# Kernel tuning notes

Hardware: AMD Instinct MI355X
Metric: run time of the kernel (lower is better)

The kernel has to match this reference:

```python
import jax, jax.numpy as jnp
import numpy as np
import math

B, W, BINS, BANDS = 2, 2048, 1024, 8  # cropsize == W
HEAD = BINS // BANDS


def setup_inputs() -> dict:
    key = jax.random.key(0)
    ks = jax.random.split(key, 10)
    s = 1.0 / math.sqrt(BINS)
    return {
        "x": jax.random.normal(ks[0], (B, W, BINS), jnp.float32),
        "Wq": jax.random.normal(ks[1], (BINS, BINS), jnp.float32) * s,
        "bq": jax.random.normal(ks[2], (BINS,), jnp.float32) * s,
        "Wk": jax.random.normal(ks[3], (BINS, BINS), jnp.float32) * s,
        "bk": jax.random.normal(ks[4], (BINS,), jnp.float32) * s,
        "Wv": jax.random.normal(ks[5], (BINS, BINS), jnp.float32) * s,
        "bv": jax.random.normal(ks[6], (BINS,), jnp.float32) * s,
        "Wo": jax.random.normal(ks[7], (BINS, BINS), jnp.float32) * s,
        "bo": jax.random.normal(ks[8], (BINS,), jnp.float32) * s,
        "er": jax.random.normal(ks[9], (HEAD, W), jnp.float32) * s,  # [bins//num_bands, cropsize]
    }


def reference(x, Wq, bq, Wk, bk, Wv, bv, Wo, bo, er):
    b, w, h = x.shape
    n = BANDS
    # projections -> [b, n, w, head]
    q = (x @ Wq.T + bq).reshape(b, w, n, -1).transpose(0, 2, 1, 3)
    k = (x @ Wk.T + bk).reshape(b, w, n, -1).transpose(0, 2, 1, 3)
    v = (x @ Wv.T + bv).reshape(b, w, n, -1).transpose(0, 2, 1, 3)
    # relative position bias via skew trick: [b, n, w, cropsize]
    qer = jnp.einsum('bnwd,dc->bnwc', q, er)
    p = jnp.pad(qer, ((0, 0), (0, 0), (0, 0), (1, 0)))  # pad left of last dim
    p = jnp.swapaxes(p, 2, 3)[:, :, 1:, :]              # [b, n, w, w]
    a = (jnp.einsum('bnqd,bnkd->bnqk', q, k) + p) / math.sqrt(h)
    attn = jax.nn.softmax(a, axis=-1)
    ctx = jnp.einsum('bnqk,bnkd->bnqd', attn, v).transpose(0, 2, 1, 3).reshape(b, w, h)
    o = ctx @ Wo.T + bo
    return (o, a)
```

## Files before the change

### kernel.cpp

```cpp
#include <hip/hip_runtime.h>

typedef __attribute__((ext_vector_type(8))) __bf16 bf16x8;
typedef __attribute__((ext_vector_type(4))) float f32x4;

__device__ __forceinline__ unsigned short f2bf(float f) {
  __bf16 h = (__bf16)f;
  return __builtin_bit_cast(unsigned short, h);
}

__device__ __forceinline__ f32x4 mfma_bf16(bf16x8 a, bf16x8 b, f32x4 c) {
  return __builtin_amdgcn_mfma_f32_16x16x32_bf16(a, b, c, 0, 0, 0);
}

__device__ __forceinline__ void gload_lds16(const void* g, void* l) {
  __builtin_amdgcn_global_load_lds((const __attribute__((address_space(1))) void*)g,
                                   (__attribute__((address_space(3))) void*)l, 16, 0, 0);
}


__global__ void cvt_f32_bf16(const float* __restrict__ in, unsigned short* __restrict__ out, int n4) {
  int i = blockIdx.x * blockDim.x + threadIdx.x;
  if (i < n4) {
    float4 v = reinterpret_cast<const float4*>(in)[i];
    ushort4 o;
    o.x = f2bf(v.x); o.y = f2bf(v.y); o.z = f2bf(v.z); o.w = f2bf(v.w);
    reinterpret_cast<ushort4*>(out)[i] = o;
  }
}

__global__ void cvt4_f32_bf16(const float* __restrict__ a, const float* __restrict__ b,
                              const float* __restrict__ c, const float* __restrict__ d,
                              unsigned short* __restrict__ oa, unsigned short* __restrict__ ob,
                              unsigned short* __restrict__ oc, unsigned short* __restrict__ od) {
  int i = blockIdx.x * blockDim.x + threadIdx.x;
  int which = i >> 18, j = i & 262143;
  const float* src = (which == 0) ? a : (which == 1) ? b : (which == 2) ? c : d;
  unsigned short* dst = (which == 0) ? oa : (which == 1) ? ob : (which == 2) ? oc : od;
  float4 v = reinterpret_cast<const float4*>(src)[j];
  ushort4 o;
  o.x = f2bf(v.x); o.y = f2bf(v.y); o.z = f2bf(v.z); o.w = f2bf(v.w);
  reinterpret_cast<ushort4*>(dst)[j] = o;
}

__global__ void er_transpose(const float* __restrict__ er, unsigned short* __restrict__ ert) {
  __shared__ float t[32][33];
  int w0 = blockIdx.x * 32, d0 = blockIdx.y * 32;
  int tx = threadIdx.x, ty = threadIdx.y;
#pragma unroll
  for (int i = 0; i < 4; ++i)
    t[ty + i * 8][tx] = er[(size_t)(d0 + ty + i * 8) * 2048 + w0 + tx];
  __syncthreads();
#pragma unroll
  for (int i = 0; i < 4; ++i)
    ert[(size_t)(w0 + ty + i * 8) * 128 + d0 + tx] = f2bf(t[tx][ty + i * 8]);
}


__device__ __forceinline__ void gemm_tile(
    const unsigned short* __restrict__ A,
    const unsigned short* __restrict__ Bt,
    const float* __restrict__ bias,
    void* __restrict__ C,
    int mode, int i0, int j0,
    unsigned short* lds)
{
  char* base = (char*)lds;

  const int tid = threadIdx.x;
  const int lane = tid & 63, wid = tid >> 6;
  const int lr = lane & 15, lq = lane >> 4;
  const int wr = wid >> 1, wc = wid & 1;

  f32x4 acc[4][4] = {};

  const int srow = tid >> 2;
  const int scolb = (tid & 3) << 4;

  const char* Abase = (const char*)A + (size_t)(i0 + srow) * 2048 + scolb;
  const char* Bbase = (const char*)Bt + (size_t)(j0 + srow) * 2048 + scolb;

  gload_lds16(Abase,             base + tid * 16);
  gload_lds16(Abase + 64 * 2048, base + 4096 + tid * 16);
  gload_lds16(Bbase,             base + 8192 + tid * 16);
  gload_lds16(Bbase + 64 * 2048, base + 12288 + tid * 16);

  for (int kt = 0; kt < 32; ++kt) {
    char* cbuf = base + (kt & 1) * 16384;
    char* nbuf = base + ((kt + 1) & 1) * 16384;

    asm volatile("s_waitcnt vmcnt(0)" ::: "memory");
    __builtin_amdgcn_sched_barrier(0);
    __builtin_amdgcn_s_barrier();
    __builtin_amdgcn_sched_barrier(0);

    if (kt < 31) {
      const int k0b = (kt + 1) * 64;
      gload_lds16(Abase + k0b,             nbuf + tid * 16);
      gload_lds16(Abase + k0b + 64 * 2048, nbuf + 4096 + tid * 16);
      gload_lds16(Bbase + k0b,             nbuf + 8192 + tid * 16);
      gload_lds16(Bbase + k0b + 64 * 2048, nbuf + 12288 + tid * 16);
    }
    __builtin_amdgcn_sched_barrier(0);

    bf16x8 af[4], bfr[4];
#pragma unroll
    for (int m = 0; m < 4; ++m)
      af[m] = *(const bf16x8*)(cbuf + (wr * 64 + m * 16 + lr) * 64 + lq * 16);
#pragma unroll
    for (int n = 0; n < 4; ++n)
      bfr[n] = *(const bf16x8*)(cbuf + 8192 + (wc * 64 + n * 16 + lr) * 64 + lq * 16);
    __builtin_amdgcn_s_setprio(1);
#pragma unroll
    for (int m = 0; m < 4; ++m)
#pragma unroll
      for (int n = 0; n < 4; ++n)
        acc[m][n] = mfma_bf16(af[m], bfr[n], acc[m][n]);
    __builtin_amdgcn_s_setprio(0);
  }

  float bv[4];
#pragma unroll
  for (int n = 0; n < 4; ++n) bv[n] = bias[j0 + wc * 64 + n * 16 + lr];

  if (mode == 1) {
    __syncthreads();
#pragma unroll
    for (int m = 0; m < 4; ++m)
#pragma unroll
      for (int n = 0; n < 4; ++n)
#pragma unroll
        for (int r = 0; r < 4; ++r) {
          int il = wr * 64 + m * 16 + lq * 4 + r;
          int jl = wc * 64 + n * 16 + lr;
          lds[jl * 132 + il] = f2bf(acc[m][n][r] + bv[n]);
        }
    __syncthreads();
    const int b = i0 >> 11, w0 = i0 & 2047, bd = j0 >> 7;
    unsigned short* out = (unsigned short*)C;
    for (int idx = tid; idx < 16384; idx += 256) {
      int dl = idx >> 7, wl = idx & 127;
      out[(size_t)((b * 8 + bd) * 128 + dl) * 2048 + w0 + wl] = lds[dl * 132 + wl];
    }
  } else if (mode == 0) {
    unsigned short* out = (unsigned short*)C;
#pragma unroll
    for (int m = 0; m < 4; ++m)
#pragma unroll
      for (int n = 0; n < 4; ++n)
#pragma unroll
        for (int r = 0; r < 4; ++r) {
          int gi = i0 + wr * 64 + m * 16 + lq * 4 + r;
          int gj = j0 + wc * 64 + n * 16 + lr;
          out[(size_t)gi * 1024 + gj] = f2bf(acc[m][n][r] + bv[n]);
        }
  } else {
    float* out = (float*)C;
#pragma unroll
    for (int m = 0; m < 4; ++m)
#pragma unroll
      for (int n = 0; n < 4; ++n)
#pragma unroll
        for (int r = 0; r < 4; ++r) {
          int gi = i0 + wr * 64 + m * 16 + lq * 4 + r;
          int gj = j0 + wc * 64 + n * 16 + lr;
          out[(size_t)gi * 1024 + gj] = acc[m][n][r] + bv[n];
        }
  }
}

__global__ __launch_bounds__(256, 2) void gemm_qkv(
    const unsigned short* __restrict__ xb,
    const unsigned short* __restrict__ Wqb, const unsigned short* __restrict__ Wkb,
    const unsigned short* __restrict__ Wvb,
    const float* __restrict__ bq, const float* __restrict__ bk, const float* __restrict__ bv_,
    unsigned short* __restrict__ Qb, unsigned short* __restrict__ Kb,
    unsigned short* __restrict__ Vtb)
{
  __shared__ unsigned short lds[16896];
  const int which = blockIdx.y >> 3;
  const int i0 = blockIdx.x * 128, j0 = (blockIdx.y & 7) * 128;
  const unsigned short* Bt = (which == 0) ? Wqb : (which == 1) ? Wkb : Wvb;
  const float* bias = (which == 0) ? bq : (which == 1) ? bk : bv_;
  void* C = (which == 0) ? (void*)Qb : (which == 1) ? (void*)Kb : (void*)Vtb;
  gemm_tile(xb, Bt, bias, C, (which == 2) ? 1 : 0, i0, j0, lds);
}

__global__ __launch_bounds__(256, 2) void gemm_bt(
    const unsigned short* __restrict__ A,
    const unsigned short* __restrict__ Bt,
    const float* __restrict__ bias,
    void* __restrict__ C,
    int mode)
{
  __shared__ unsigned short lds[16896];
  gemm_tile(A, Bt, bias, C, mode, blockIdx.x * 128, blockIdx.y * 128, lds);
}


__global__ __launch_bounds__(512) void attn_fused(
    const unsigned short* __restrict__ Qb,
    const unsigned short* __restrict__ Kb,
    const unsigned short* __restrict__ Vt,
    const unsigned short* __restrict__ ErT,
    float* __restrict__ a_out,
    unsigned short* __restrict__ ctx)
{
  __shared__ __align__(16) char Klb[32768];
  __shared__ __align__(16) char Qlb[32768];
  __shared__ __align__(16) char Vlb[32768];
  __shared__ __align__(16) char Plb[32768];

  const int bb = blockIdx.x;
  const int bd = bb & 7, b = bb >> 3;
  const int qi0 = blockIdx.y * 128;
  const int tid = threadIdx.x, wid = tid >> 6, lane = tid & 63;
  const int lr = lane & 15, lq = lane >> 4;

  bf16x8 qf[4], ef[4];
  {
    const unsigned short* Qrow = Qb + (size_t)(b * 2048 + qi0 + wid * 16 + lr) * 1024 + bd * 128;
    const unsigned short* Erow = ErT + (size_t)(qi0 + wid * 16 + lr) * 128;
#pragma unroll
    for (int kk = 0; kk < 4; ++kk) {
      qf[kk] = *(const bf16x8*)(Qrow + kk * 32 + lq * 8);
      ef[kk] = *(const bf16x8*)(Erow + kk * 32 + lq * 8);
    }
  }

  int ldso[4];
  const char *ksrc[4], *qsrc[4], *vsrc[4];
#pragma unroll
  for (int p = 0; p < 4; ++p) {
    int L = p * 8192 + tid * 16;
    int row = L >> 8, cs = L & 255;
    int sc = cs ^ ((row & 7) << 4);
    ldso[p] = L;
    ksrc[p] = (const char*)Kb + ((size_t)(b * 2048 + row) * 1024 + bd * 128) * 2 + sc;
    qsrc[p] = (const char*)Qb + ((size_t)(b * 2048 + row) * 1024 + bd * 128) * 2 + sc;
    vsrc[p] = (const char*)Vt + ((size_t)(bb * 128 + row) * 2048) * 2 + sc;
  }

#pragma unroll
  for (int p = 0; p < 4; ++p) gload_lds16(ksrc[p], Klb + ldso[p]);
#pragma unroll
  for (int p = 0; p < 4; ++p) gload_lds16(qsrc[p], Qlb + ldso[p]);
#pragma unroll
  for (int p = 0; p < 4; ++p) gload_lds16(vsrc[p], Vlb + ldso[p]);

  f32x4 oacc[8] = {};
  float M[4], L[4];
#pragma unroll
  for (int r = 0; r < 4; ++r) { M[r] = -1e30f; L[r] = 0.f; }

  float* abase = a_out + (size_t)bb * 2048 * 2048;

  for (int kt = 0; kt < 16; ++kt) {
    const int kj0 = kt * 128;
    const size_t nkq = (size_t)((kt + 1) & 15) * 262144;
    const size_t nv = (size_t)((kt + 1) & 15) * 256;

    asm volatile("s_waitcnt vmcnt(4)" ::: "memory");
    __builtin_amdgcn_sched_barrier(0);
    __builtin_amdgcn_s_barrier();
    __builtin_amdgcn_sched_barrier(0);

    f32x4 sacc[8] = {};
    __builtin_amdgcn_s_setprio(1);
#pragma unroll
    for (int kk = 0; kk < 4; ++kk) {
#pragma unroll
      for (int nf = 0; nf < 8; ++nf) {
        const int row = nf * 16 + lr;
        bf16x8 kf = *(const bf16x8*)(Klb + row * 256 + ((kk * 64 + lq * 16) ^ ((row & 7) << 4)));
        sacc[nf] = mfma_bf16(qf[kk], kf, sacc[nf]);
      }
#pragma unroll
      for (int nf = 0; nf < 8; ++nf) {
        const int row = nf * 16 + lr;
        bf16x8 qkf = *(const bf16x8*)(Qlb + row * 256 + ((kk * 64 + lq * 16) ^ ((row & 7) << 4)));
        sacc[nf] = mfma_bf16(ef[kk], qkf, sacc[nf]);
      }
    }
    __builtin_amdgcn_s_setprio(0);

    __builtin_amdgcn_sched_barrier(0);
    __builtin_amdgcn_s_barrier();
    __builtin_amdgcn_sched_barrier(0);

#pragma unroll
    for (int nf = 0; nf < 8; ++nf)
#pragma unroll
      for (int r = 0; r < 4; ++r) sacc[nf][r] *= 0.03125f;
    {
      const int qrow_base = qi0 + wid * 16 + lq * 4;
#pragma unroll
      for (int nf = 0; nf < 8; ++nf)
#pragma unroll
        for (int r = 0; r < 4; ++r)
          abase[(size_t)(qrow_base + r) * 2048 + kj0 + nf * 16 + lr] = sacc[nf][r];
    }

    __builtin_amdgcn_sched_barrier(0);
#pragma unroll
    for (int p = 0; p < 4; ++p) gload_lds16(ksrc[p] + nkq, Klb + ldso[p]);
#pragma unroll
    for (int p = 0; p < 4; ++p) gload_lds16(qsrc[p] + nkq, Qlb + ldso[p]);
    __builtin_amdgcn_sched_barrier(0);

    float rmax[4];
#pragma unroll
    for (int r = 0; r < 4; ++r) {
      float m0 = sacc[0][r];
#pragma unroll
      for (int nf = 1; nf < 8; ++nf) m0 = fmaxf(m0, sacc[nf][r]);
      m0 = fmaxf(m0, __shfl_xor(m0, 1));
      m0 = fmaxf(m0, __shfl_xor(m0, 2));
      m0 = fmaxf(m0, __shfl_xor(m0, 4));
      m0 = fmaxf(m0, __shfl_xor(m0, 8));
      rmax[r] = m0;
    }
    bool small = (rmax[0] - M[0] <= 8.f) & (rmax[1] - M[1] <= 8.f) &
                 (rmax[2] - M[2] <= 8.f) & (rmax[3] - M[3] <= 8.f);
    unsigned long long vote = __ballot(small);
    if (vote != ~0ull) {
      float scl[4];
#pragma unroll
      for (int r = 0; r < 4; ++r) {
        float Mn = fmaxf(M[r], rmax[r]);
        scl[r] = __expf(M[r] - Mn);
        M[r] = Mn;
        L[r] *= scl[r];
      }
#pragma unroll
      for (int dn = 0; dn < 8; ++dn)
#pragma unroll
        for (int r = 0; r < 4; ++r) oacc[dn][r] *= scl[r];
    }
    float rsum[4] = {0.f, 0.f, 0.f, 0.f};
#pragma unroll
    for (int nf = 0; nf < 8; ++nf)
#pragma unroll
      for (int r = 0; r < 4; ++r) {
        float pv = __expf(sacc[nf][r] - M[r]);
        sacc[nf][r] = pv;
        rsum[r] += pv;
      }
    {
      const int prow0 = wid * 16 + lq * 4;
#pragma unroll
      for (int nf = 0; nf < 8; ++nf)
#pragma unroll
        for (int r = 0; r < 4; ++r) {
          const int row = prow0 + r;
          *(unsigned short*)(Plb + row * 256 + (((nf * 16 + lr) * 2) ^ ((row & 7) << 4))) =
              f2bf(sacc[nf][r]);
        }
    }
#pragma unroll
    for (int r = 0; r < 4; ++r) {
      rsum[r] += __shfl_xor(rsum[r], 1);
      rsum[r] += __shfl_xor(rsum[r], 2);
      rsum[r] += __shfl_xor(rsum[r], 4);
      rsum[r] += __shfl_xor(rsum[r], 8);
      L[r] += rsum[r];
    }

    asm volatile("s_waitcnt vmcnt(8)" ::: "memory");
    __builtin_amdgcn_sched_barrier(0);

    __builtin_amdgcn_s_setprio(1);
#pragma unroll
    for (int kk = 0; kk < 4; ++kk) {
      const int prow = wid * 16 + lr;
      bf16x8 pf = *(const bf16x8*)(Plb + prow * 256 + ((kk * 64 + lq * 16) ^ ((prow & 7) << 4)));
#pragma unroll
      for (int dn = 0; dn < 8; ++dn) {
        const int vrow = dn * 16 + lr;
        bf16x8 vf = *(const bf16x8*)(Vlb + vrow * 256 + ((kk * 64 + lq * 16) ^ ((vrow & 7) << 4)));
        oacc[dn] = mfma_bf16(pf, vf, oacc[dn]);
      }
    }
    __builtin_amdgcn_s_setprio(0);

    __builtin_amdgcn_sched_barrier(0);
    __builtin_amdgcn_s_barrier();
    __builtin_amdgcn_sched_barrier(0);
#pragma unroll
    for (int p = 0; p < 4; ++p) gload_lds16(vsrc[p] + nv, Vlb + ldso[p]);
    __builtin_amdgcn_sched_barrier(0);
  }

  {
    const int qrow_base = b * 2048 + qi0 + wid * 16 + lq * 4;
#pragma unroll
    for (int dn = 0; dn < 8; ++dn)
#pragma unroll
      for (int r = 0; r < 4; ++r) {
        float v = oacc[dn][r] / L[r];
        ctx[(size_t)(qrow_base + r) * 1024 + bd * 128 + dn * 16 + lr] = f2bf(v);
      }
  }
}


extern "C" void kernel_launch(void* const* d_in, const int* in_sizes, int n_in,
                              void* d_out, int out_size, void* d_ws, size_t ws_size,
                              hipStream_t stream) {
  const float* x  = (const float*)d_in[0];
  const float* Wq = (const float*)d_in[1];
  const float* bq = (const float*)d_in[2];
  const float* Wk = (const float*)d_in[3];
  const float* bk = (const float*)d_in[4];
  const float* Wv = (const float*)d_in[5];
  const float* bv = (const float*)d_in[6];
  const float* Wo = (const float*)d_in[7];
  const float* bo = (const float*)d_in[8];
  const float* er = (const float*)d_in[9];

  char* ws = (char*)d_ws;
  unsigned short* xb  = (unsigned short*)(ws + 0);
  unsigned short* Wqb = (unsigned short*)(ws + 8388608);
  unsigned short* Wkb = (unsigned short*)(ws + 10485760);
  unsigned short* Wvb = (unsigned short*)(ws + 12582912);
  unsigned short* Wob = (unsigned short*)(ws + 14680064);
  unsigned short* Qb  = (unsigned short*)(ws + 16777216);
  unsigned short* Kb  = (unsigned short*)(ws + 25165824);
  unsigned short* Vtb = (unsigned short*)(ws + 33554432);
  unsigned short* ctx = (unsigned short*)(ws + 41943040);
  unsigned short* ert = (unsigned short*)(ws + 50331648);

  float* a_out = (float*)d_out + 4194304;

  cvt_f32_bf16<<<dim3(4096), dim3(256), 0, stream>>>(x, xb, 1048576);
  cvt4_f32_bf16<<<dim3(4096), dim3(256), 0, stream>>>(Wq, Wk, Wv, Wo, Wqb, Wkb, Wvb, Wob);
  er_transpose<<<dim3(64, 4), dim3(32, 8), 0, stream>>>(er, ert);

  gemm_qkv<<<dim3(32, 24), dim3(256), 0, stream>>>(xb, Wqb, Wkb, Wvb, bq, bk, bv,
                                                   Qb, Kb, Vtb);

  attn_fused<<<dim3(16, 16), dim3(512), 0, stream>>>(Qb, Kb, Vtb, ert, a_out, ctx);

  gemm_bt<<<dim3(32, 8), dim3(256), 0, stream>>>(ctx, Wob, bo, d_out, 2);
}
```

Before: 188.6 us.

## Fuse Q/K/V projections into one GEMM kernel sharing the x tile

Replaces the 768-block QKV GEMM, which reloaded the same x tile three times, with a 256-block kernel. Each block loads one x tile and computes the Q, K and V accumulators together, using a 128-wide K step, XOR-swizzled LDS and 128 KB of shared memory. This is meant to cut redundant global and LDS traffic for the activation operand and raise MFMA work per load. In exchange it holds 48 accumulator tiles per thread and runs at one block per CU, and 256 blocks may underfill the 256 CUs, so occupancy and latency hiding could suffer.

```diff
diff --git a/kernel.cpp b/kernel.cpp
--- a/kernel.cpp
+++ b/kernel.cpp
@@ -56,28 +56,159 @@
 }
 
 
-__device__ __forceinline__ void gemm_tile(
-    const unsigned short* __restrict__ A,
-    const unsigned short* __restrict__ Bt,
-    const float* __restrict__ bias,
-    void* __restrict__ C,
-    int mode, int i0, int j0,
-    unsigned short* lds)
+__global__ __launch_bounds__(256, 1) void gemm_qkv3(
+    const unsigned short* __restrict__ xb,
+    const unsigned short* __restrict__ Wqb, const unsigned short* __restrict__ Wkb,
+    const unsigned short* __restrict__ Wvb,
+    const float* __restrict__ bq, const float* __restrict__ bk, const float* __restrict__ bvv,
+    unsigned short* __restrict__ Qb, unsigned short* __restrict__ Kb,
+    unsigned short* __restrict__ Vtb)
 {
-  char* base = (char*)lds;
+  __shared__ __align__(16) char lds[131072];
 
   const int tid = threadIdx.x;
   const int lane = tid & 63, wid = tid >> 6;
   const int lr = lane & 15, lq = lane >> 4;
   const int wr = wid >> 1, wc = wid & 1;
+  const int i0 = blockIdx.x * 128, j0 = blockIdx.y * 128;
+
+  f32x4 aQ[4][4] = {}, aK[4][4] = {}, aV[4][4] = {};
+
+  int ldso[4];
+  const char *asrc[4], *qsrc[4], *ksrc[4], *vsrc[4];
+#pragma unroll
+  for (int p = 0; p < 4; ++p) {
+    int L = p * 4096 + tid * 16;
+    int row = L >> 7, colb = L & 127;
+    int sc = colb ^ ((row & 7) << 4);
+    ldso[p] = L;
+    asrc[p] = (const char*)xb  + (size_t)(i0 + row) * 2048 + sc;
+    qsrc[p] = (const char*)Wqb + (size_t)(j0 + row) * 2048 + sc;
+    ksrc[p] = (const char*)Wkb + (size_t)(j0 + row) * 2048 + sc;
+    vsrc[p] = (const char*)Wvb + (size_t)(j0 + row) * 2048 + sc;
+  }
+
+#pragma unroll
+  for (int p = 0; p < 4; ++p) gload_lds16(asrc[p], lds + ldso[p]);
+#pragma unroll
+  for (int p = 0; p < 4; ++p) gload_lds16(qsrc[p], lds + 16384 + ldso[p]);
+#pragma unroll
+  for (int p = 0; p < 4; ++p) gload_lds16(ksrc[p], lds + 32768 + ldso[p]);
+#pragma unroll
+  for (int p = 0; p < 4; ++p) gload_lds16(vsrc[p], lds + 49152 + ldso[p]);
+
+  const int swz = (lr & 7) << 4;
+
+  for (int kt = 0; kt < 16; ++kt) {
+    char* cb = lds + (kt & 1) * 65536;
+    char* nb = lds + ((kt + 1) & 1) * 65536;
+
+    asm volatile("s_waitcnt vmcnt(0)" ::: "memory");
+    __builtin_amdgcn_sched_barrier(0);
+    __builtin_amdgcn_s_barrier();
+    __builtin_amdgcn_sched_barrier(0);
+
+    if (kt < 15) {
+      const int k0b = (kt + 1) * 128;
+#pragma unroll
+      for (int p = 0; p < 4; ++p) gload_lds16(asrc[p] + k0b, nb + ldso[p]);
+#pragma unroll
+      for (int p = 0; p < 4; ++p) gload_lds16(qsrc[p] + k0b, nb + 16384 + ldso[p]);
+#pragma unroll
+      for (int p = 0; p < 4; ++p) gload_lds16(ksrc[p] + k0b, nb + 32768 + ldso[p]);
+#pragma unroll
+      for (int p = 0; p < 4; ++p) gload_lds16(vsrc[p] + k0b, nb + 49152 + ldso[p]);
+    }
+    __builtin_amdgcn_sched_barrier(0);
+
+#pragma unroll
+    for (int kk = 0; kk < 2; ++kk) {
+      const int coff = (kk * 64 + lq * 16) ^ swz;
+      bf16x8 af[4];
+#pragma unroll
+      for (int m = 0; m < 4; ++m)
+        af[m] = *(const bf16x8*)(cb + (wr * 64 + m * 16 + lr) * 128 + coff);
+      bf16x8 bq_[4], bk_[4], bv_[4];
+#pragma unroll
+      for (int n = 0; n < 4; ++n) {
+        const int rb = (wc * 64 + n * 16 + lr) * 128 + coff;
+        bq_[n] = *(const bf16x8*)(cb + 16384 + rb);
+        bk_[n] = *(const bf16x8*)(cb + 32768 + rb);
+        bv_[n] = *(const bf16x8*)(cb + 49152 + rb);
+      }
+      __builtin_amdgcn_s_setprio(1);
+#pragma unroll
+      for (int m = 0; m < 4; ++m)
+#pragma unroll
+        for (int n = 0; n < 4; ++n) {
+          aQ[m][n] = mfma_bf16(af[m], bq_[n], aQ[m][n]);
+          aK[m][n] = mfma_bf16(af[m], bk_[n], aK[m][n]);
+          aV[m][n] = mfma_bf16(af[m], bv_[n], aV[m][n]);
+        }
+      __builtin_amdgcn_s_setprio(0);
+    }
+  }
+
+  float vbq[4], vbk[4], vbv[4];
+#pragma unroll
+  for (int n = 0; n < 4; ++n) {
+    int gj = j0 + wc * 64 + n * 16 + lr;
+    vbq[n] = bq[gj]; vbk[n] = bk[gj]; vbv[n] = bvv[gj];
+  }
+
+#pragma unroll
+  for (int m = 0; m < 4; ++m)
+#pragma unroll
+    for (int n = 0; n < 4; ++n)
+#pragma unroll
+      for (int r = 0; r < 4; ++r) {
+        int gi = i0 + wr * 64 + m * 16 + lq * 4 + r;
+        int gj = j0 + wc * 64 + n * 16 + lr;
+        Qb[(size_t)gi * 1024 + gj] = f2bf(aQ[m][n][r] + vbq[n]);
+        Kb[(size_t)gi * 1024 + gj] = f2bf(aK[m][n][r] + vbk[n]);
+      }
+
+  __syncthreads();
+  unsigned short* lds16 = (unsigned short*)lds;
+#pragma unroll
+  for (int m = 0; m < 4; ++m)
+#pragma unroll
+    for (int n = 0; n < 4; ++n)
+#pragma unroll
+      for (int r = 0; r < 4; ++r) {
+        int il = wr * 64 + m * 16 + lq * 4 + r;
+        int jl = wc * 64 + n * 16 + lr;
+        lds16[jl * 132 + il] = f2bf(aV[m][n][r] + vbv[n]);
+      }
+  __syncthreads();
+  {
+    const int b = i0 >> 11, w0 = i0 & 2047, bd = j0 >> 7;
+    for (int idx = tid; idx < 16384; idx += 256) {
+      int dl = idx >> 7, wl = idx & 127;
+      Vtb[(size_t)((b * 8 + bd) * 128 + dl) * 2048 + w0 + wl] = lds16[dl * 132 + wl];
+    }
+  }
+}
+
+
+__global__ __launch_bounds__(256, 2) void gemm_bt(
+    const unsigned short* __restrict__ A,
+    const unsigned short* __restrict__ Bt,
+    const float* __restrict__ bias,
+    float* __restrict__ C)
+{
+  __shared__ __align__(16) char base[32768];
+
+  const int tid = threadIdx.x;
+  const int lane = tid & 63, wid = tid >> 6;
+  const int lr = lane & 15, lq = lane >> 4;
+  const int wr = wid >> 1, wc = wid & 1;
+  const int i0 = blockIdx.x * 128, j0 = blockIdx.y * 128;
 
   f32x4 acc[4][4] = {};
 
-  const int srow = tid >> 2;
-  const int scolb = (tid & 3) << 4;
-
-  const char* Abase = (const char*)A + (size_t)(i0 + srow) * 2048 + scolb;
-  const char* Bbase = (const char*)Bt + (size_t)(j0 + srow) * 2048 + scolb;
+  const char* Abase = (const char*)A + (size_t)(i0 + (tid >> 2)) * 2048 + ((tid & 3) << 4);
+  const char* Bbase = (const char*)Bt + (size_t)(j0 + (tid >> 2)) * 2048 + ((tid & 3) << 4);
 
   gload_lds16(Abase,             base + tid * 16);
   gload_lds16(Abase + 64 * 2048, base + 4096 + tid * 16);
@@ -121,79 +252,16 @@
   float bv[4];
 #pragma unroll
   for (int n = 0; n < 4; ++n) bv[n] = bias[j0 + wc * 64 + n * 16 + lr];
-
-  if (mode == 1) {
-    __syncthreads();
-#pragma unroll
-    for (int m = 0; m < 4; ++m)
-#pragma unroll
-      for (int n = 0; n < 4; ++n)
-#pragma unroll
-        for (int r = 0; r < 4; ++r) {
-          int il = wr * 64 + m * 16 + lq * 4 + r;
-          int jl = wc * 64 + n * 16 + lr;
-          lds[jl * 132 + il] = f2bf(acc[m][n][r] + bv[n]);
-        }
-    __syncthreads();
-    const int b = i0 >> 11, w0 = i0 & 2047, bd = j0 >> 7;
-    unsigned short* out = (unsigned short*)C;
-    for (int idx = tid; idx < 16384; idx += 256) {
-      int dl = idx >> 7, wl = idx & 127;
-      out[(size_t)((b * 8 + bd) * 128 + dl) * 2048 + w0 + wl] = lds[dl * 132 + wl];
-    }
-  } else if (mode == 0) {
-    unsigned short* out = (unsigned short*)C;
-#pragma unroll
-    for (int m = 0; m < 4; ++m)
-#pragma unroll
-      for (int n = 0; n < 4; ++n)
-#pragma unroll
-        for (int r = 0; r < 4; ++r) {
-          int gi = i0 + wr * 64 + m * 16 + lq * 4 + r;
-          int gj = j0 + wc * 64 + n * 16 + lr;
-          out[(size_t)gi * 1024 + gj] = f2bf(acc[m][n][r] + bv[n]);
-        }
-  } else {
-    float* out = (float*)C;
-#pragma unroll
-    for (int m = 0; m < 4; ++m)
-#pragma unroll
-      for (int n = 0; n < 4; ++n)
-#pragma unroll
-        for (int r = 0; r < 4; ++r) {
-          int gi = i0 + wr * 64 + m * 16 + lq * 4 + r;
-          int gj = j0 + wc * 64 + n * 16 + lr;
-          out[(size_t)gi * 1024 + gj] = acc[m][n][r] + bv[n];
-        }
-  }
-}
-
-__global__ __launch_bounds__(256, 2) void gemm_qkv(
-    const unsigned short* __restrict__ xb,
-    const unsigned short* __restrict__ Wqb, const unsigned short* __restrict__ Wkb,
-    const unsigned short* __restrict__ Wvb,
-    const float* __restrict__ bq, const float* __restrict__ bk, const float* __restrict__ bv_,
-    unsigned short* __restrict__ Qb, unsigned short* __restrict__ Kb,
-    unsigned short* __restrict__ Vtb)
-{
-  __shared__ unsigned short lds[16896];
-  const int which = blockIdx.y >> 3;
-  const int i0 = blockIdx.x * 128, j0 = (blockIdx.y & 7) * 128;
-  const unsigned short* Bt = (which == 0) ? Wqb : (which == 1) ? Wkb : Wvb;
-  const float* bias = (which == 0) ? bq : (which == 1) ? bk : bv_;
-  void* C = (which == 0) ? (void*)Qb : (which == 1) ? (void*)Kb : (void*)Vtb;
-  gemm_tile(xb, Bt, bias, C, (which == 2) ? 1 : 0, i0, j0, lds);
-}
-
-__global__ __launch_bounds__(256, 2) void gemm_bt(
-    const unsigned short* __restrict__ A,
-    const unsigned short* __restrict__ Bt,
-    const float* __restrict__ bias,
-    void* __restrict__ C,
-    int mode)
-{
-  __shared__ unsigned short lds[16896];
-  gemm_tile(A, Bt, bias, C, mode, blockIdx.x * 128, blockIdx.y * 128, lds);
+#pragma unroll
+  for (int m = 0; m < 4; ++m)
+#pragma unroll
+    for (int n = 0; n < 4; ++n)
+#pragma unroll
+      for (int r = 0; r < 4; ++r) {
+        int gi = i0 + wr * 64 + m * 16 + lq * 4 + r;
+        int gj = j0 + wc * 64 + n * 16 + lr;
+        C[(size_t)gi * 1024 + gj] = acc[m][n][r] + bv[n];
+      }
 }
 
 
@@ -435,10 +503,10 @@
   cvt4_f32_bf16<<<dim3(4096), dim3(256), 0, stream>>>(Wq, Wk, Wv, Wo, Wqb, Wkb, Wvb, Wob);
   er_transpose<<<dim3(64, 4), dim3(32, 8), 0, stream>>>(er, ert);
 
-  gemm_qkv<<<dim3(32, 24), dim3(256), 0, stream>>>(xb, Wqb, Wkb, Wvb, bq, bk, bv,
+  gemm_qkv3<<<dim3(32, 8), dim3(256), 0, stream>>>(xb, Wqb, Wkb, Wvb, bq, bk, bv,
                                                    Qb, Kb, Vtb);
 
   attn_fused<<<dim3(16, 16), dim3(512), 0, stream>>>(Qb, Kb, Vtb, ert, a_out, ctx);
 
-  gemm_bt<<<dim3(32, 8), dim3(256), 0, stream>>>(ctx, Wob, bo, d_out, 2);
-}
+  gemm_bt<<<dim3(32, 8), dim3(256), 0, stream>>>(ctx, Wob, bo, (float*)d_out);
+}
```

New measurement: 189.9 us. About the same (+0.7%).
